# Kernel tuning notes

Measured on AMD Instinct MI355X. Metric: run time of the kernel, lower is better.

The kernel has to match this reference:

```python
import jax, jax.numpy as jnp
import numpy as np

B, S_Q, S_KV, DIM, H = 2, 2048, 2048, 1024, 16
HD = DIM // H
SCALE = HD ** -0.5
EPS = 1e-8


def apply_rope(x, freqs):
    # x: (b, s, h, hd); freqs: (b, s, hd) = [cos | sin] halves of size hd//2
    xr = x.reshape(x.shape[:-1] + (HD // 2, 2))
    x_r, x_i = xr[..., 0], xr[..., 1]
    cos, sin = jnp.split(freqs, 2, axis=-1)          # each (b, s, hd//2)
    cos = cos[:, :, None, :]
    sin = sin[:, :, None, :]
    o_r = x_r * cos - x_i * sin
    o_i = x_r * sin + x_i * cos
    return jnp.stack([o_r, o_i], axis=-1).reshape(x.shape)


def setup_inputs() -> dict:
    key = jax.random.key(0)
    ks = jax.random.split(key, 9)
    q_x = jax.random.normal(ks[0], (B, S_Q, DIM), jnp.float32)
    kv_x = jax.random.normal(ks[1], (B, S_KV, DIM), jnp.float32)
    q_freqs_cis = jax.random.normal(ks[2], (B, S_Q, HD), jnp.float32)
    k_freqs_cis = jax.random.normal(ks[3], (B, S_KV, HD), jnp.float32)
    mask = jnp.zeros((B, 1, S_Q, S_KV), jnp.float32)
    attn_prior = jax.random.uniform(ks[4], (B, S_Q, S_KV), jnp.float32)
    Wq = jax.random.normal(ks[5], (DIM, DIM), jnp.float32) * 0.02
    Wkv = jax.random.normal(ks[6], (2 * DIM, DIM), jnp.float32) * 0.02
    Wproj = jax.random.normal(ks[7], (DIM, DIM), jnp.float32) * 0.02
    bproj = jax.random.normal(ks[8], (DIM,), jnp.float32) * 0.02
    return {"q_x": q_x, "kv_x": kv_x, "q_freqs_cis": q_freqs_cis,
            "k_freqs_cis": k_freqs_cis, "mask": mask, "attn_prior": attn_prior,
            "Wq": Wq, "Wkv": Wkv, "Wproj": Wproj, "bproj": bproj}


def reference(q_x, kv_x, q_freqs_cis, k_freqs_cis, mask, attn_prior,
              Wq, Wkv, Wproj, bproj):
    b, sq, _ = q_x.shape
    skv = kv_x.shape[1]
    q = (q_x @ Wq.T).reshape(b, sq, H, HD)
    kv = (kv_x @ Wkv.T).reshape(b, skv, 2, H, HD)
    k, v = kv[:, :, 0], kv[:, :, 1]
    q = apply_rope(q, q_freqs_cis)
    k = apply_rope(k, k_freqs_cis)
    # scores: (b, h, q, k)
    attn = jnp.einsum("bqhd,bkhd->bhqk", q * SCALE, k)
    attn = attn + mask
    attn = jax.nn.softmax(attn, axis=-1)
    # log-space fusion with multiplicative prior, then renormalize
    prior = attn_prior[:, None, :, :]
    attn = jnp.exp(jnp.log(jnp.clip(attn, EPS)) + jnp.log(jnp.clip(prior, EPS)))
    attn = attn / jnp.sum(attn, axis=-1, keepdims=True)
    x = jnp.einsum("bhqk,bkhd->bqhd", attn, v).reshape(b, sq, DIM)
    x = x @ Wproj.T + bproj
    return (x, attn)
```

## Files before the change

kernel.cpp:

```cpp
#include <hip/hip_runtime.h>
#include <hip/hip_bf16.h>

typedef __bf16 bf16;
typedef __bf16 bf16x4 __attribute__((ext_vector_type(4)));
typedef __bf16 bf16x8 __attribute__((ext_vector_type(8)));
typedef float floatx4 __attribute__((ext_vector_type(4)));
typedef float float4v __attribute__((ext_vector_type(4)));

#define MFMA16(a, b, c) __builtin_amdgcn_mfma_f32_16x16x32_bf16(a, b, c, 0, 0, 0)

constexpr int B_ = 2, S_ = 2048, DIM_ = 1024, H_ = 16, HD_ = 64;
constexpr float SCALE_ = 0.125f;
constexpr float EPS_ = 1e-8f;

__device__ __forceinline__ void gload_lds16(const void* g, void* l) {
    __builtin_amdgcn_global_load_lds(
        (const __attribute__((address_space(1))) void*)g,
        (__attribute__((address_space(3))) void*)l, 16, 0, 0);
}

__global__ __launch_bounds__(256) void cvt_kernel(const float* __restrict__ in,
                                                  bf16* __restrict__ out, int n4) {
    int i = blockIdx.x * 256 + threadIdx.x;
    if (i >= n4) return;
    float4v v = ((const float4v*)in)[i];
    bf16x4 o;
    o[0] = (bf16)v[0]; o[1] = (bf16)v[1]; o[2] = (bf16)v[2]; o[3] = (bf16)v[3];
    ((bf16x4*)out)[i] = o;
}

__global__ __launch_bounds__(256) void lp_kernel(const float* __restrict__ mask,
                                                 const float* __restrict__ prior,
                                                 float* __restrict__ lp, int n4) {
    int i = blockIdx.x * 256 + threadIdx.x;
    if (i >= n4) return;
    float4v m = ((const float4v*)mask)[i];
    float4v p = ((const float4v*)prior)[i];
    float4v o;
#pragma unroll
    for (int j = 0; j < 4; ++j) o[j] = m[j] + __logf(fmaxf(p[j], EPS_));
    ((float4v*)lp)[i] = o;
}

template<int OUTF32, int BIASED>
__global__ __launch_bounds__(256) void gemm_bt(const bf16* __restrict__ A,
                                               const bf16* __restrict__ B,
                                               void* __restrict__ Cp,
                                               const float* __restrict__ bias,
                                               int M, int N, int K) {
    __shared__ bf16 As[128 * 64];
    __shared__ bf16 Bs[128 * 64];
    const int lane = threadIdx.x & 63, wid = threadIdx.x >> 6;
    const int colL = lane & 15, grp = lane >> 4;
    const int bm = blockIdx.y * 128, bn = blockIdx.x * 128;
    const int wr = wid >> 1, wc = wid & 1;

    floatx4 acc[4][4];
#pragma unroll
    for (int m = 0; m < 4; ++m)
#pragma unroll
        for (int n = 0; n < 4; ++n) acc[m][n] = (floatx4){0.f, 0.f, 0.f, 0.f};

    for (int k0 = 0; k0 < K; k0 += 64) {
#pragma unroll
        for (int i = 0; i < 4; ++i) {
            int c = wid * 256 + i * 64 + lane;
            int row = c >> 3, sub = c & 7;
            gload_lds16(A + (size_t)(bm + row) * K + k0 + sub * 8,
                        &As[(wid * 256 + i * 64) * 8]);
            gload_lds16(B + (size_t)(bn + row) * K + k0 + sub * 8,
                        &Bs[(wid * 256 + i * 64) * 8]);
        }
        __syncthreads();
#pragma unroll
        for (int ks = 0; ks < 2; ++ks) {
            bf16x8 af[4], bfr[4];
#pragma unroll
            for (int m = 0; m < 4; ++m)
                af[m] = *(const bf16x8*)(&As[(wr * 64 + m * 16 + colL) * 64 + ks * 32 + grp * 8]);
#pragma unroll
            for (int n = 0; n < 4; ++n)
                bfr[n] = *(const bf16x8*)(&Bs[(wc * 64 + n * 16 + colL) * 64 + ks * 32 + grp * 8]);
#pragma unroll
            for (int m = 0; m < 4; ++m)
#pragma unroll
                for (int n = 0; n < 4; ++n)
                    acc[m][n] = MFMA16(af[m], bfr[n], acc[m][n]);
        }
        __syncthreads();
    }

#pragma unroll
    for (int m = 0; m < 4; ++m)
#pragma unroll
        for (int n = 0; n < 4; ++n)
#pragma unroll
            for (int r = 0; r < 4; ++r) {
                int row = bm + wr * 64 + m * 16 + grp * 4 + r;
                int col = bn + wc * 64 + n * 16 + colL;
                float v = acc[m][n][r];
                if (BIASED) v += bias[col];
                if (OUTF32) ((float*)Cp)[(size_t)row * N + col] = v;
                else        ((bf16*)Cp)[(size_t)row * N + col] = (bf16)v;
            }
}

__global__ __launch_bounds__(256) void rope_kernel(const bf16* __restrict__ in,
                                                   const float* __restrict__ fr,
                                                   bf16* __restrict__ out,
                                                   int in_ld, float scale) {
    int tid = blockIdx.x * 256 + threadIdx.x;
    int j = tid & 7, h = (tid >> 3) & 15, s = (tid >> 7) & 2047, b = tid >> 18;
    bf16x8 x = *(const bf16x8*)(in + (size_t)(b * 2048 + s) * in_ld + h * 64 + j * 8);
    const float* f = fr + (size_t)(b * 2048 + s) * 64 + j * 4;
    bf16x8 o;
#pragma unroll
    for (int i = 0; i < 4; ++i) {
        float c = f[i], sn = f[32 + i];
        float x0 = (float)x[2 * i], x1 = (float)x[2 * i + 1];
        o[2 * i]     = (bf16)((x0 * c - x1 * sn) * scale);
        o[2 * i + 1] = (bf16)((x0 * sn + x1 * c) * scale);
    }
    *(bf16x8*)(out + ((size_t)(b * 16 + h) * 2048 + s) * 64 + j * 8) = o;
}

__global__ __launch_bounds__(256) void vtrans_kernel(const bf16* __restrict__ KVp,
                                                     bf16* __restrict__ Vt) {
    int bid = blockIdx.x;
    int sb = bid & 31, h = (bid >> 5) & 15, b = bid >> 9;
    __shared__ bf16 tile[64][66];
    int tid = threadIdx.x;
#pragma unroll
    for (int i = 0; i < 2; ++i) {
        int c = tid + i * 256;
        int row = c >> 3, sub = c & 7;
        bf16x8 x = *(const bf16x8*)(KVp + (size_t)(b * 2048 + sb * 64 + row) * 2048
                                    + 1024 + h * 64 + sub * 8);
#pragma unroll
        for (int k = 0; k < 8; ++k) tile[row][sub * 8 + k] = x[k];
    }
    __syncthreads();
#pragma unroll
    for (int i = 0; i < 2; ++i) {
        int c = tid + i * 256;
        int drow = c >> 3, sub = c & 7;
        bf16x8 o;
#pragma unroll
        for (int k = 0; k < 8; ++k) o[k] = tile[sub * 8 + k][drow];
        *(bf16x8*)(Vt + ((size_t)(b * 16 + h) * 64 + drow) * 2048 + sb * 64 + sub * 8) = o;
    }
}

__global__ __launch_bounds__(256) void attn_fused(const bf16* __restrict__ Qr,
                                                  const bf16* __restrict__ Kr,
                                                  const bf16* __restrict__ Vt,
                                                  const float* __restrict__ lp,
                                                  float* __restrict__ attn_out,
                                                  bf16* __restrict__ O) {
    __shared__ bf16 KB[2][4096];
    __shared__ float LP[2][4096];
    union ShU {
        struct { bf16 VB[2][4096]; bf16 P[4][1024]; } p1;
        float FS[4][1088];
    };
    __shared__ ShU Ush;

    const int tid = threadIdx.x;
    const int lane = tid & 63, wv = tid >> 6;
    const int colL = lane & 15, grp = lane >> 4;
    const int n = blockIdx.x;
    const int x = n & 7, j = n >> 3;
    const int h = j & 15;
    const int pp = (j >> 4) * 8 + x;
    const int b = pp >> 5, qb = pp & 31;
    const int bh = b * H_ + h;
    const int q0 = qb * 64 + wv * 16;
    const int rowL = wv * 16 + colL;

    const bf16* Qbase = Qr + ((size_t)bh * S_ + q0) * HD_;
    const bf16* Kbase = Kr + (size_t)bh * S_ * HD_;
    const bf16* Vbase = Vt + (size_t)bh * HD_ * S_;
    const float* LPbase = lp + ((size_t)b * S_ + qb * 64) * S_;

    bf16x8 qf0 = *(const bf16x8*)(Qbase + (size_t)colL * HD_ + grp * 8);
    bf16x8 qf1 = *(const bf16x8*)(Qbase + (size_t)colL * HD_ + 32 + grp * 8);

    bf16* P = Ush.p1.P[wv];
    const int swz = (colL & 7) << 3;
    const int c7 = colL & 7;

    auto stageK = [&](int buf, int k0) {
#pragma unroll
        for (int i = 0; i < 2; ++i) {
            int c = i * 256 + tid;
            int row = c >> 3, sub = c & 7;
            gload_lds16(Kbase + (size_t)(k0 + row) * HD_ + ((sub ^ (row & 7)) << 3),
                        &KB[buf][(c & ~63) << 3]);
        }
    };
    auto stageV = [&](int buf, int k0) {
#pragma unroll
        for (int i = 0; i < 2; ++i) {
            int c = i * 256 + tid;
            int row = c >> 3, sub = c & 7;
            gload_lds16(Vbase + (size_t)row * S_ + k0 + ((sub ^ (row & 7)) << 3),
                        &Ush.p1.VB[buf][(c & ~63) << 3]);
        }
    };
    auto stageLP = [&](int buf, int k0) {
#pragma unroll
        for (int i = 0; i < 4; ++i) {
            int c = i * 256 + tid;
            int row = c >> 4, col16 = c & 15;
            gload_lds16(LPbase + (size_t)row * S_ + k0 + ((col16 ^ (row & 7)) << 2),
                        &LP[buf][(c & ~63) << 2]);
        }
    };
    auto lpAddr = [&](int ct) {
        return rowL * 64 + (((ct * 4 + grp) ^ (rowL & 7)) << 2);
    };

    float ua = 0.f;
    floatx4 oT[4];
#pragma unroll
    for (int dt = 0; dt < 4; ++dt) oT[dt] = (floatx4){0.f, 0.f, 0.f, 0.f};

    stageK(0, 0);
    stageV(0, 0);
    stageLP(0, 0);
    __syncthreads();

    for (int kt = 0; kt < 32; ++kt) {
        const int k0 = kt * 64;
        const int cur = kt & 1;
        if (kt < 31) {
            stageK(cur ^ 1, k0 + 64);
            stageV(cur ^ 1, k0 + 64);
            stageLP(cur ^ 1, k0 + 64);
        }

        floatx4 s[4];
#pragma unroll
        for (int ct = 0; ct < 4; ++ct) {
            const int r8 = (ct * 16 + colL) * 8;
            bf16x8 a0 = *(const bf16x8*)&KB[cur][(r8 + (grp ^ c7)) * 8];
            bf16x8 a1 = *(const bf16x8*)&KB[cur][(r8 + (grp ^ 4 ^ c7)) * 8];
            floatx4 acc = (floatx4){0.f, 0.f, 0.f, 0.f};
            acc = MFMA16(a0, qf0, acc);
            acc = MFMA16(a1, qf1, acc);
            s[ct] = acc;
        }
#pragma unroll
        for (int ct = 0; ct < 4; ++ct) {
            float4v lv = *(const float4v*)&LP[cur][lpAddr(ct)];
            bf16x4 pw;
#pragma unroll
            for (int r = 0; r < 4; ++r) {
                float tv = __expf(s[ct][r] + lv[r]);
                ua += tv;
                pw[r] = (bf16)tv;
            }
            *(bf16x4*)&P[(colL * 64 + ct * 16 + grp * 4) ^ swz] = pw;
        }
#pragma unroll
        for (int ks = 0; ks < 2; ++ks) {
            bf16x8 pb = *(const bf16x8*)&P[(colL * 64 + ks * 32 + grp * 8) ^ swz];
#pragma unroll
            for (int dt = 0; dt < 4; ++dt) {
                const int r8 = (dt * 16 + colL) * 8;
                bf16x8 vf = *(const bf16x8*)&Ush.p1.VB[cur][(r8 + ((ks * 4 + grp) ^ c7)) * 8];
                oT[dt] = MFMA16(vf, pb, oT[dt]);
            }
        }
        __syncthreads();
    }

    ua += __shfl_xor(ua, 16, 64);
    ua += __shfl_xor(ua, 32, 64);
    const float iu = 1.0f / ua;
#pragma unroll
    for (int dt = 0; dt < 4; ++dt) {
        bf16x4 ow;
#pragma unroll
        for (int r = 0; r < 4; ++r) ow[r] = (bf16)(oT[dt][r] * iu);
        *(bf16x4*)(O + ((size_t)b * S_ + q0 + colL) * DIM_ + h * HD_ + dt * 16 + grp * 4) = ow;
    }

    __syncthreads();
    stageK(0, 0);
    stageLP(0, 0);
    __syncthreads();

    const float* Aout = attn_out + (size_t)bh * S_ * S_;
    for (int kt = 0; kt < 32; ++kt) {
        const int k0 = kt * 64;
        const int cur = kt & 1;
        if (kt < 31) {
            stageK(cur ^ 1, k0 + 64);
            stageLP(cur ^ 1, k0 + 64);
        }

        floatx4 s[4];
#pragma unroll
        for (int ct = 0; ct < 4; ++ct) {
            const int r8 = (ct * 16 + colL) * 8;
            bf16x8 a0 = *(const bf16x8*)&KB[cur][(r8 + (grp ^ c7)) * 8];
            bf16x8 a1 = *(const bf16x8*)&KB[cur][(r8 + (grp ^ 4 ^ c7)) * 8];
            floatx4 acc = (floatx4){0.f, 0.f, 0.f, 0.f};
            acc = MFMA16(a0, qf0, acc);
            acc = MFMA16(a1, qf1, acc);
            s[ct] = acc;
        }
#pragma unroll
        for (int ct = 0; ct < 4; ++ct) {
            float4v lv = *(const float4v*)&LP[cur][lpAddr(ct)];
            float4v o;
#pragma unroll
            for (int r = 0; r < 4; ++r)
                o[r] = __expf(s[ct][r] + lv[r]) * iu;
            *(float4v*)&Ush.FS[wv][colL * 68 + ct * 16 + grp * 4] = o;
        }
#pragma unroll
        for (int it = 0; it < 4; ++it) {
            const int row = it * 4 + grp;
            float4v v = *(const float4v*)&Ush.FS[wv][row * 68 + colL * 4];
            *(float4v*)(Aout + (size_t)(q0 + row) * S_ + k0 + colL * 4) = v;
        }
        __syncthreads();
    }
}

extern "C" void kernel_launch(void* const* d_in, const int* in_sizes, int n_in,
                              void* d_out, int out_size, void* d_ws, size_t ws_size,
                              hipStream_t stream) {
    const float* q_x   = (const float*)d_in[0];
    const float* kv_x  = (const float*)d_in[1];
    const float* q_fr  = (const float*)d_in[2];
    const float* k_fr  = (const float*)d_in[3];
    const float* maskp = (const float*)d_in[4];
    const float* prior = (const float*)d_in[5];
    const float* Wq    = (const float*)d_in[6];
    const float* Wkv   = (const float*)d_in[7];
    const float* Wproj = (const float*)d_in[8];
    const float* bproj = (const float*)d_in[9];

    float* out_x    = (float*)d_out;
    float* out_attn = out_x + (size_t)B_ * S_ * DIM_;

    char* w = (char*)d_ws;
    bf16* qx_b  = (bf16*)(w + (size_t)0);
    bf16* kvx_b = (bf16*)(w + ((size_t)8  << 20));
    bf16* wq_b  = (bf16*)(w + ((size_t)16 << 20));
    bf16* wkv_b = (bf16*)(w + ((size_t)18 << 20));
    bf16* wpj_b = (bf16*)(w + ((size_t)22 << 20));
    bf16* qp    = (bf16*)(w + ((size_t)24 << 20));
    bf16* kvp   = (bf16*)(w + ((size_t)32 << 20));
    bf16* qr    = (bf16*)(w + ((size_t)48 << 20));
    bf16* kr    = (bf16*)(w + ((size_t)56 << 20));
    bf16* vt    = (bf16*)(w + ((size_t)64 << 20));
    bf16* ob    = (bf16*)(w + ((size_t)72 << 20));
    float* lpb  = (float*)(w + ((size_t)96 << 20));

    cvt_kernel<<<4096, 256, 0, stream>>>(q_x,   qx_b,  1048576);
    cvt_kernel<<<4096, 256, 0, stream>>>(kv_x,  kvx_b, 1048576);
    cvt_kernel<<<1024, 256, 0, stream>>>(Wq,    wq_b,   262144);
    cvt_kernel<<<2048, 256, 0, stream>>>(Wkv,   wkv_b,  524288);
    cvt_kernel<<<1024, 256, 0, stream>>>(Wproj, wpj_b,  262144);
    lp_kernel<<<8192, 256, 0, stream>>>(maskp, prior, lpb, 2097152);

    gemm_bt<0, 0><<<dim3(8, 32),  256, 0, stream>>>(qx_b,  wq_b,  qp,  nullptr, 4096, 1024, 1024);
    gemm_bt<0, 0><<<dim3(16, 32), 256, 0, stream>>>(kvx_b, wkv_b, kvp, nullptr, 4096, 2048, 1024);

    rope_kernel<<<2048, 256, 0, stream>>>(qp,  q_fr, qr, 1024, SCALE_);
    rope_kernel<<<2048, 256, 0, stream>>>(kvp, k_fr, kr, 2048, 1.0f);
    vtrans_kernel<<<1024, 256, 0, stream>>>(kvp, vt);

    attn_fused<<<1024, 256, 0, stream>>>(qr, kr, vt, lpb, out_attn, ob);

    gemm_bt<1, 1><<<dim3(8, 32), 256, 0, stream>>>(ob, wpj_b, out_x, bproj, 4096, 1024, 1024);
}
```

Baseline: 417.4 us.

## Use 512-thread attention blocks with half-tile log-prior staging and single-buffered K

Each attention block now covers 128 query rows with 8 waves instead of 64 rows with 4 waves, so every K/V tile staged into LDS is shared by twice as many query rows. The log-prior tile is split into two 32-column halves that are prefetched at different points in the iteration. K becomes single-buffered and is refilled after a mid-iteration barrier, which lowers LDS use. The per-tile work is cut into two halves with an extra barrier each, and the FS scratch buffer now uses an XOR swizzle in place of padding. The added barriers and tighter register budget under launch_bounds(512,4) could reduce latency hiding.

```diff
diff --git a/kernel.cpp b/kernel.cpp
--- a/kernel.cpp
+++ b/kernel.cpp
@@ -151,19 +151,19 @@
     }
 }
 
-__global__ __launch_bounds__(256) void attn_fused(const bf16* __restrict__ Qr,
-                                                  const bf16* __restrict__ Kr,
-                                                  const bf16* __restrict__ Vt,
-                                                  const float* __restrict__ lp,
-                                                  float* __restrict__ attn_out,
-                                                  bf16* __restrict__ O) {
-    __shared__ bf16 KB[2][4096];
-    __shared__ float LP[2][4096];
+__global__ __launch_bounds__(512, 4) void attn_fused(const bf16* __restrict__ Qr,
+                                                     const bf16* __restrict__ Kr,
+                                                     const bf16* __restrict__ Vt,
+                                                     const float* __restrict__ lp,
+                                                     float* __restrict__ attn_out,
+                                                     bf16* __restrict__ O) {
+    __shared__ bf16 KB[4096];
+    __shared__ float LPH[2][4096];
     union ShU {
-        struct { bf16 VB[2][4096]; bf16 P[4][1024]; } p1;
-        float FS[4][1088];
-    };
-    __shared__ ShU Ush;
+        struct { bf16 VB[2][4096]; bf16 P[8][1024]; } p1;
+        float FS[8][1024];
+    };
+    __shared__ ShU sm;
 
     const int tid = threadIdx.x;
     const int lane = tid & 63, wv = tid >> 6;
@@ -172,87 +172,80 @@
     const int x = n & 7, j = n >> 3;
     const int h = j & 15;
     const int pp = (j >> 4) * 8 + x;
-    const int b = pp >> 5, qb = pp & 31;
+    const int b = pp >> 4, qt = pp & 15;
     const int bh = b * H_ + h;
-    const int q0 = qb * 64 + wv * 16;
+    const int q0 = qt * 128 + wv * 16;
     const int rowL = wv * 16 + colL;
 
     const bf16* Qbase = Qr + ((size_t)bh * S_ + q0) * HD_;
     const bf16* Kbase = Kr + (size_t)bh * S_ * HD_;
     const bf16* Vbase = Vt + (size_t)bh * HD_ * S_;
-    const float* LPbase = lp + ((size_t)b * S_ + qb * 64) * S_;
+    const float* LPbase = lp + ((size_t)b * S_ + qt * 128) * S_;
 
     bf16x8 qf0 = *(const bf16x8*)(Qbase + (size_t)colL * HD_ + grp * 8);
     bf16x8 qf1 = *(const bf16x8*)(Qbase + (size_t)colL * HD_ + 32 + grp * 8);
 
-    bf16* P = Ush.p1.P[wv];
+    bf16* P = sm.p1.P[wv];
     const int swz = (colL & 7) << 3;
     const int c7 = colL & 7;
-
-    auto stageK = [&](int buf, int k0) {
+    const int r7 = rowL & 7;
+
+    auto stageK = [&](int k0) {
+        int c = tid, row = c >> 3, sub = c & 7;
+        gload_lds16(Kbase + (size_t)(k0 + row) * HD_ + ((sub ^ (row & 7)) << 3),
+                    &KB[(c & ~63) << 3]);
+    };
+    auto stageV = [&](int buf, int k0) {
+        int c = tid, row = c >> 3, sub = c & 7;
+        gload_lds16(Vbase + (size_t)row * S_ + k0 + ((sub ^ (row & 7)) << 3),
+                    &sm.p1.VB[buf][(c & ~63) << 3]);
+    };
+    auto stageLPH = [&](int buf, int k0h) {
 #pragma unroll
         for (int i = 0; i < 2; ++i) {
-            int c = i * 256 + tid;
-            int row = c >> 3, sub = c & 7;
-            gload_lds16(Kbase + (size_t)(k0 + row) * HD_ + ((sub ^ (row & 7)) << 3),
-                        &KB[buf][(c & ~63) << 3]);
-        }
-    };
-    auto stageV = [&](int buf, int k0) {
-#pragma unroll
-        for (int i = 0; i < 2; ++i) {
-            int c = i * 256 + tid;
-            int row = c >> 3, sub = c & 7;
-            gload_lds16(Vbase + (size_t)row * S_ + k0 + ((sub ^ (row & 7)) << 3),
-                        &Ush.p1.VB[buf][(c & ~63) << 3]);
-        }
-    };
-    auto stageLP = [&](int buf, int k0) {
-#pragma unroll
-        for (int i = 0; i < 4; ++i) {
-            int c = i * 256 + tid;
-            int row = c >> 4, col16 = c & 15;
-            gload_lds16(LPbase + (size_t)row * S_ + k0 + ((col16 ^ (row & 7)) << 2),
-                        &LP[buf][(c & ~63) << 2]);
-        }
-    };
-    auto lpAddr = [&](int ct) {
-        return rowL * 64 + (((ct * 4 + grp) ^ (rowL & 7)) << 2);
-    };
-
-    float ua = 0.f;
-    floatx4 oT[4];
-#pragma unroll
-    for (int dt = 0; dt < 4; ++dt) oT[dt] = (floatx4){0.f, 0.f, 0.f, 0.f};
-
-    stageK(0, 0);
-    stageV(0, 0);
-    stageLP(0, 0);
-    __syncthreads();
-
-    for (int kt = 0; kt < 32; ++kt) {
-        const int k0 = kt * 64;
-        const int cur = kt & 1;
-        if (kt < 31) {
-            stageK(cur ^ 1, k0 + 64);
-            stageV(cur ^ 1, k0 + 64);
-            stageLP(cur ^ 1, k0 + 64);
-        }
-
-        floatx4 s[4];
+            int c = i * 512 + tid, row = c >> 3, ch = c & 7;
+            gload_lds16(LPbase + (size_t)row * S_ + k0h + ((ch ^ (row & 7)) << 2),
+                        &LPH[buf][(c & ~63) << 2]);
+        }
+    };
+    auto lpRead = [&](int ct) -> float4v {
+        int lch = ((ct & 1) * 4 + grp) ^ r7;
+        return *(const float4v*)&LPH[ct >> 1][rowL * 32 + (lch << 2)];
+    };
+    auto qk = [&](floatx4* s) {
 #pragma unroll
         for (int ct = 0; ct < 4; ++ct) {
             const int r8 = (ct * 16 + colL) * 8;
-            bf16x8 a0 = *(const bf16x8*)&KB[cur][(r8 + (grp ^ c7)) * 8];
-            bf16x8 a1 = *(const bf16x8*)&KB[cur][(r8 + (grp ^ 4 ^ c7)) * 8];
+            bf16x8 a0 = *(const bf16x8*)&KB[(r8 + (grp ^ c7)) * 8];
+            bf16x8 a1 = *(const bf16x8*)&KB[(r8 + (grp ^ 4 ^ c7)) * 8];
             floatx4 acc = (floatx4){0.f, 0.f, 0.f, 0.f};
             acc = MFMA16(a0, qf0, acc);
             acc = MFMA16(a1, qf1, acc);
             s[ct] = acc;
         }
-#pragma unroll
-        for (int ct = 0; ct < 4; ++ct) {
-            float4v lv = *(const float4v*)&LP[cur][lpAddr(ct)];
+    };
+
+    float ua = 0.f;
+    floatx4 oT[4];
+#pragma unroll
+    for (int dt = 0; dt < 4; ++dt) oT[dt] = (floatx4){0.f, 0.f, 0.f, 0.f};
+
+    stageK(0);
+    stageV(0, 0);
+    stageLPH(0, 0);
+    __syncthreads();
+    stageLPH(1, 32);
+
+    for (int kt = 0; kt < 32; ++kt) {
+        const int k0 = kt * 64;
+        const int cur = kt & 1;
+
+        floatx4 s[4];
+        qk(s);
+
+#pragma unroll
+        for (int ct = 0; ct < 2; ++ct) {
+            float4v lv = lpRead(ct);
             bf16x4 pw;
 #pragma unroll
             for (int r = 0; r < 4; ++r) {
@@ -262,17 +255,41 @@
             }
             *(bf16x4*)&P[(colL * 64 + ct * 16 + grp * 4) ^ swz] = pw;
         }
-#pragma unroll
-        for (int ks = 0; ks < 2; ++ks) {
-            bf16x8 pb = *(const bf16x8*)&P[(colL * 64 + ks * 32 + grp * 8) ^ swz];
+        {
+            bf16x8 pb = *(const bf16x8*)&P[(colL * 64 + grp * 8) ^ swz];
 #pragma unroll
             for (int dt = 0; dt < 4; ++dt) {
                 const int r8 = (dt * 16 + colL) * 8;
-                bf16x8 vf = *(const bf16x8*)&Ush.p1.VB[cur][(r8 + ((ks * 4 + grp) ^ c7)) * 8];
+                bf16x8 vf = *(const bf16x8*)&sm.p1.VB[cur][(r8 + (grp ^ c7)) * 8];
                 oT[dt] = MFMA16(vf, pb, oT[dt]);
             }
         }
         __syncthreads();
+        if (kt < 31) { stageLPH(0, k0 + 64); stageK(k0 + 64); stageV(cur ^ 1, k0 + 64); }
+
+#pragma unroll
+        for (int ct = 2; ct < 4; ++ct) {
+            float4v lv = lpRead(ct);
+            bf16x4 pw;
+#pragma unroll
+            for (int r = 0; r < 4; ++r) {
+                float tv = __expf(s[ct][r] + lv[r]);
+                ua += tv;
+                pw[r] = (bf16)tv;
+            }
+            *(bf16x4*)&P[(colL * 64 + ct * 16 + grp * 4) ^ swz] = pw;
+        }
+        {
+            bf16x8 pb = *(const bf16x8*)&P[(colL * 64 + 32 + grp * 8) ^ swz];
+#pragma unroll
+            for (int dt = 0; dt < 4; ++dt) {
+                const int r8 = (dt * 16 + colL) * 8;
+                bf16x8 vf = *(const bf16x8*)&sm.p1.VB[cur][(r8 + ((4 + grp) ^ c7)) * 8];
+                oT[dt] = MFMA16(vf, pb, oT[dt]);
+            }
+        }
+        __syncthreads();
+        if (kt < 31) stageLPH(1, k0 + 96);
     }
 
     ua += __shfl_xor(ua, 16, 64);
@@ -286,47 +303,45 @@
         *(bf16x4*)(O + ((size_t)b * S_ + q0 + colL) * DIM_ + h * HD_ + dt * 16 + grp * 4) = ow;
     }
 
+    stageK(0);
+    stageLPH(0, 0);
     __syncthreads();
-    stageK(0, 0);
-    stageLP(0, 0);
-    __syncthreads();
+    stageLPH(1, 32);
 
     const float* Aout = attn_out + (size_t)bh * S_ * S_;
     for (int kt = 0; kt < 32; ++kt) {
         const int k0 = kt * 64;
-        const int cur = kt & 1;
-        if (kt < 31) {
-            stageK(cur ^ 1, k0 + 64);
-            stageLP(cur ^ 1, k0 + 64);
-        }
 
         floatx4 s[4];
-#pragma unroll
-        for (int ct = 0; ct < 4; ++ct) {
-            const int r8 = (ct * 16 + colL) * 8;
-            bf16x8 a0 = *(const bf16x8*)&KB[cur][(r8 + (grp ^ c7)) * 8];
-            bf16x8 a1 = *(const bf16x8*)&KB[cur][(r8 + (grp ^ 4 ^ c7)) * 8];
-            floatx4 acc = (floatx4){0.f, 0.f, 0.f, 0.f};
-            acc = MFMA16(a0, qf0, acc);
-            acc = MFMA16(a1, qf1, acc);
-            s[ct] = acc;
-        }
-#pragma unroll
-        for (int ct = 0; ct < 4; ++ct) {
-            float4v lv = *(const float4v*)&LP[cur][lpAddr(ct)];
+        qk(s);
+
+#pragma unroll
+        for (int ct = 0; ct < 2; ++ct) {
+            float4v lv = lpRead(ct);
             float4v o;
 #pragma unroll
-            for (int r = 0; r < 4; ++r)
-                o[r] = __expf(s[ct][r] + lv[r]) * iu;
-            *(float4v*)&Ush.FS[wv][colL * 68 + ct * 16 + grp * 4] = o;
+            for (int r = 0; r < 4; ++r) o[r] = __expf(s[ct][r] + lv[r]) * iu;
+            *(float4v*)&sm.FS[wv][colL * 64 + ((ct * 16 + grp * 4) ^ swz)] = o;
+        }
+        __syncthreads();
+        if (kt < 31) { stageLPH(0, k0 + 64); stageK(k0 + 64); }
+
+#pragma unroll
+        for (int ct = 2; ct < 4; ++ct) {
+            float4v lv = lpRead(ct);
+            float4v o;
+#pragma unroll
+            for (int r = 0; r < 4; ++r) o[r] = __expf(s[ct][r] + lv[r]) * iu;
+            *(float4v*)&sm.FS[wv][colL * 64 + ((ct * 16 + grp * 4) ^ swz)] = o;
         }
 #pragma unroll
         for (int it = 0; it < 4; ++it) {
             const int row = it * 4 + grp;
-            float4v v = *(const float4v*)&Ush.FS[wv][row * 68 + colL * 4];
+            float4v v = *(const float4v*)&sm.FS[wv][row * 64 + ((colL * 4) ^ ((row & 7) << 3))];
             *(float4v*)(Aout + (size_t)(q0 + row) * S_ + k0 + colL * 4) = v;
         }
         __syncthreads();
+        if (kt < 31) stageLPH(1, k0 + 96);
     }
 }
 
@@ -375,7 +390,7 @@
     rope_kernel<<<2048, 256, 0, stream>>>(kvp, k_fr, kr, 2048, 1.0f);
     vtrans_kernel<<<1024, 256, 0, stream>>>(kvp, vt);
 
-    attn_fused<<<1024, 256, 0, stream>>>(qr, kr, vt, lpb, out_attn, ob);
+    attn_fused<<<512, 512, 0, stream>>>(qr, kr, vt, lpb, out_attn, ob);
 
     gemm_bt<1, 1><<<dim3(8, 32), 256, 0, stream>>>(ob, wpj_b, out_x, bproj, 4096, 1024, 1024);
 }
```

Result: slower. 436.5 us (+4.6%).

## Store log-prior in bf16, load V straight to registers, raise occupancy

Applied to the files above, without the earlier changes.

The log(prior)+mask buffer is now written and read as bf16 instead of fp32, which halves its HBM traffic in both the lp_kernel and the two attention passes, and also halves its LDS staging. V tiles are no longer staged through LDS; each wave loads its V fragments from global memory into registers. This frees shared memory, and launch bounds now request 3 blocks per CU. The cost is reduced precision of the log-prior added before exp, which affects the attention output, plus register pressure from the V fragments and uncoalesced strided global V loads.

```diff
diff --git a/kernel.cpp b/kernel.cpp
--- a/kernel.cpp
+++ b/kernel.cpp
@@ -31,15 +31,15 @@
 
 __global__ __launch_bounds__(256) void lp_kernel(const float* __restrict__ mask,
                                                  const float* __restrict__ prior,
-                                                 float* __restrict__ lp, int n4) {
+                                                 bf16* __restrict__ lp, int n4) {
     int i = blockIdx.x * 256 + threadIdx.x;
     if (i >= n4) return;
     float4v m = ((const float4v*)mask)[i];
     float4v p = ((const float4v*)prior)[i];
-    float4v o;
-#pragma unroll
-    for (int j = 0; j < 4; ++j) o[j] = m[j] + __logf(fmaxf(p[j], EPS_));
-    ((float4v*)lp)[i] = o;
+    bf16x4 o;
+#pragma unroll
+    for (int j = 0; j < 4; ++j) o[j] = (bf16)(m[j] + __logf(fmaxf(p[j], EPS_)));
+    ((bf16x4*)lp)[i] = o;
 }
 
 template<int OUTF32, int BIASED>
@@ -151,19 +151,19 @@
     }
 }
 
-__global__ __launch_bounds__(256) void attn_fused(const bf16* __restrict__ Qr,
-                                                  const bf16* __restrict__ Kr,
-                                                  const bf16* __restrict__ Vt,
-                                                  const float* __restrict__ lp,
-                                                  float* __restrict__ attn_out,
-                                                  bf16* __restrict__ O) {
+__global__ __launch_bounds__(256, 3) void attn_fused(const bf16* __restrict__ Qr,
+                                                     const bf16* __restrict__ Kr,
+                                                     const bf16* __restrict__ Vt,
+                                                     const bf16* __restrict__ lp,
+                                                     float* __restrict__ attn_out,
+                                                     bf16* __restrict__ O) {
     __shared__ bf16 KB[2][4096];
-    __shared__ float LP[2][4096];
+    __shared__ bf16 LPB[2][4096];
     union ShU {
-        struct { bf16 VB[2][4096]; bf16 P[4][1024]; } p1;
+        bf16 P[4][1024];
         float FS[4][1088];
     };
-    __shared__ ShU Ush;
+    __shared__ ShU sm;
 
     const int tid = threadIdx.x;
     const int lane = tid & 63, wv = tid >> 6;
@@ -180,14 +180,15 @@
     const bf16* Qbase = Qr + ((size_t)bh * S_ + q0) * HD_;
     const bf16* Kbase = Kr + (size_t)bh * S_ * HD_;
     const bf16* Vbase = Vt + (size_t)bh * HD_ * S_;
-    const float* LPbase = lp + ((size_t)b * S_ + qb * 64) * S_;
+    const bf16* LPbase = lp + ((size_t)b * S_ + qb * 64) * S_;
 
     bf16x8 qf0 = *(const bf16x8*)(Qbase + (size_t)colL * HD_ + grp * 8);
     bf16x8 qf1 = *(const bf16x8*)(Qbase + (size_t)colL * HD_ + 32 + grp * 8);
 
-    bf16* P = Ush.p1.P[wv];
+    bf16* P = sm.P[wv];
     const int swz = (colL & 7) << 3;
     const int c7 = colL & 7;
+    const int r7 = rowL & 7;
 
     auto stageK = [&](int buf, int k0) {
 #pragma unroll
@@ -198,48 +199,24 @@
                         &KB[buf][(c & ~63) << 3]);
         }
     };
-    auto stageV = [&](int buf, int k0) {
+    auto stageLP = [&](int buf, int k0) {
 #pragma unroll
         for (int i = 0; i < 2; ++i) {
             int c = i * 256 + tid;
             int row = c >> 3, sub = c & 7;
-            gload_lds16(Vbase + (size_t)row * S_ + k0 + ((sub ^ (row & 7)) << 3),
-                        &Ush.p1.VB[buf][(c & ~63) << 3]);
-        }
-    };
-    auto stageLP = [&](int buf, int k0) {
-#pragma unroll
-        for (int i = 0; i < 4; ++i) {
-            int c = i * 256 + tid;
-            int row = c >> 4, col16 = c & 15;
-            gload_lds16(LPbase + (size_t)row * S_ + k0 + ((col16 ^ (row & 7)) << 2),
-                        &LP[buf][(c & ~63) << 2]);
-        }
-    };
-    auto lpAddr = [&](int ct) {
-        return rowL * 64 + (((ct * 4 + grp) ^ (rowL & 7)) << 2);
-    };
-
-    float ua = 0.f;
-    floatx4 oT[4];
-#pragma unroll
-    for (int dt = 0; dt < 4; ++dt) oT[dt] = (floatx4){0.f, 0.f, 0.f, 0.f};
-
-    stageK(0, 0);
-    stageV(0, 0);
-    stageLP(0, 0);
-    __syncthreads();
-
-    for (int kt = 0; kt < 32; ++kt) {
-        const int k0 = kt * 64;
-        const int cur = kt & 1;
-        if (kt < 31) {
-            stageK(cur ^ 1, k0 + 64);
-            stageV(cur ^ 1, k0 + 64);
-            stageLP(cur ^ 1, k0 + 64);
-        }
-
-        floatx4 s[4];
+            gload_lds16(LPbase + (size_t)row * S_ + k0 + ((sub ^ (row & 7)) << 3),
+                        &LPB[buf][(c & ~63) << 3]);
+        }
+    };
+    auto lpRead = [&](int cur, int ct) -> float4v {
+        int chunk = ct * 2 + (grp >> 1);
+        bf16x4 v = *(const bf16x4*)&LPB[cur][rowL * 64 + ((chunk ^ r7) << 3) + ((grp & 1) << 2)];
+        float4v f;
+#pragma unroll
+        for (int r = 0; r < 4; ++r) f[r] = (float)v[r];
+        return f;
+    };
+    auto qk = [&](floatx4* s, int cur) {
 #pragma unroll
         for (int ct = 0; ct < 4; ++ct) {
             const int r8 = (ct * 16 + colL) * 8;
@@ -250,9 +227,36 @@
             acc = MFMA16(a1, qf1, acc);
             s[ct] = acc;
         }
+    };
+
+    float ua = 0.f;
+    floatx4 oT[4];
+#pragma unroll
+    for (int dt = 0; dt < 4; ++dt) oT[dt] = (floatx4){0.f, 0.f, 0.f, 0.f};
+
+    stageK(0, 0);
+    stageLP(0, 0);
+    __syncthreads();
+
+    for (int kt = 0; kt < 32; ++kt) {
+        const int k0 = kt * 64;
+        const int cur = kt & 1;
+        if (kt < 31) { stageK(cur ^ 1, k0 + 64); stageLP(cur ^ 1, k0 + 64); }
+
+        bf16x8 vf[2][4];
+#pragma unroll
+        for (int ks = 0; ks < 2; ++ks)
+#pragma unroll
+            for (int dt = 0; dt < 4; ++dt)
+                vf[ks][dt] = *(const bf16x8*)(Vbase + (size_t)(dt * 16 + colL) * S_
+                                              + k0 + ks * 32 + grp * 8);
+
+        floatx4 s[4];
+        qk(s, cur);
+
 #pragma unroll
         for (int ct = 0; ct < 4; ++ct) {
-            float4v lv = *(const float4v*)&LP[cur][lpAddr(ct)];
+            float4v lv = lpRead(cur, ct);
             bf16x4 pw;
 #pragma unroll
             for (int r = 0; r < 4; ++r) {
@@ -266,11 +270,8 @@
         for (int ks = 0; ks < 2; ++ks) {
             bf16x8 pb = *(const bf16x8*)&P[(colL * 64 + ks * 32 + grp * 8) ^ swz];
 #pragma unroll
-            for (int dt = 0; dt < 4; ++dt) {
-                const int r8 = (dt * 16 + colL) * 8;
-                bf16x8 vf = *(const bf16x8*)&Ush.p1.VB[cur][(r8 + ((ks * 4 + grp) ^ c7)) * 8];
-                oT[dt] = MFMA16(vf, pb, oT[dt]);
-            }
+            for (int dt = 0; dt < 4; ++dt)
+                oT[dt] = MFMA16(vf[ks][dt], pb, oT[dt]);
         }
         __syncthreads();
     }
@@ -286,7 +287,6 @@
         *(bf16x4*)(O + ((size_t)b * S_ + q0 + colL) * DIM_ + h * HD_ + dt * 16 + grp * 4) = ow;
     }
 
-    __syncthreads();
     stageK(0, 0);
     stageLP(0, 0);
     __syncthreads();
@@ -295,35 +295,23 @@
     for (int kt = 0; kt < 32; ++kt) {
         const int k0 = kt * 64;
         const int cur = kt & 1;
-        if (kt < 31) {
-            stageK(cur ^ 1, k0 + 64);
-            stageLP(cur ^ 1, k0 + 64);
-        }
+        if (kt < 31) { stageK(cur ^ 1, k0 + 64); stageLP(cur ^ 1, k0 + 64); }
 
         floatx4 s[4];
+        qk(s, cur);
+
 #pragma unroll
         for (int ct = 0; ct < 4; ++ct) {
-            const int r8 = (ct * 16 + colL) * 8;
-            bf16x8 a0 = *(const bf16x8*)&KB[cur][(r8 + (grp ^ c7)) * 8];
-            bf16x8 a1 = *(const bf16x8*)&KB[cur][(r8 + (grp ^ 4 ^ c7)) * 8];
-            floatx4 acc = (floatx4){0.f, 0.f, 0.f, 0.f};
-            acc = MFMA16(a0, qf0, acc);
-            acc = MFMA16(a1, qf1, acc);
-            s[ct] = acc;
-        }
-#pragma unroll
-        for (int ct = 0; ct < 4; ++ct) {
-            float4v lv = *(const float4v*)&LP[cur][lpAddr(ct)];
+            float4v lv = lpRead(cur, ct);
             float4v o;
 #pragma unroll
-            for (int r = 0; r < 4; ++r)
-                o[r] = __expf(s[ct][r] + lv[r]) * iu;
-            *(float4v*)&Ush.FS[wv][colL * 68 + ct * 16 + grp * 4] = o;
+            for (int r = 0; r < 4; ++r) o[r] = __expf(s[ct][r] + lv[r]) * iu;
+            *(float4v*)&sm.FS[wv][colL * 68 + ct * 16 + grp * 4] = o;
         }
 #pragma unroll
         for (int it = 0; it < 4; ++it) {
             const int row = it * 4 + grp;
-            float4v v = *(const float4v*)&Ush.FS[wv][row * 68 + colL * 4];
+            float4v v = *(const float4v*)&sm.FS[wv][row * 68 + colL * 4];
             *(float4v*)(Aout + (size_t)(q0 + row) * S_ + k0 + colL * 4) = v;
         }
         __syncthreads();
@@ -359,7 +347,7 @@
     bf16* kr    = (bf16*)(w + ((size_t)56 << 20));
     bf16* vt    = (bf16*)(w + ((size_t)64 << 20));
     bf16* ob    = (bf16*)(w + ((size_t)72 << 20));
-    float* lpb  = (float*)(w + ((size_t)96 << 20));
+    bf16* lpb   = (bf16*)(w + ((size_t)96 << 20));
 
     cvt_kernel<<<4096, 256, 0, stream>>>(q_x,   qx_b,  1048576);
     cvt_kernel<<<4096, 256, 0, stream>>>(kv_x,  kvx_b, 1048576);
```

Measured after the change: 484.4 us. 1.16x slower.
